# Performance work log

Measured on AMD Instinct MI355X. Metric: run time of the kernel, lower is better.

Reference implementation:

```python
import jax, jax.numpy as jnp
import numpy as np

DEPTH = 128
NEG_MAX = -jnp.finfo(jnp.float32).max


def setup_inputs() -> dict:
    key = jax.random.key(0)
    ks = jax.random.split(key, 10)
    B, S, F, C = 16, 2048, 512, 1000
    x = jax.random.normal(ks[0], (B, S, F), dtype=jnp.float32)
    attention_mask = jax.random.randint(ks[1], (B, S, S), 0, 2) == 1
    s = 1.0 / np.sqrt(F)
    Wq = jax.random.uniform(ks[2], (F, DEPTH), jnp.float32, -s, s)
    bq = jax.random.uniform(ks[3], (DEPTH,), jnp.float32, -s, s)
    Wk = jax.random.uniform(ks[4], (F, DEPTH), jnp.float32, -s, s)
    bk = jax.random.uniform(ks[5], (DEPTH,), jnp.float32, -s, s)
    Wv = jax.random.uniform(ks[6], (F, DEPTH), jnp.float32, -s, s)
    bv = jax.random.uniform(ks[7], (DEPTH,), jnp.float32, -s, s)
    sl = 1.0 / np.sqrt(DEPTH)
    Wl = jax.random.uniform(ks[8], (DEPTH, C), jnp.float32, -sl, sl)
    bl = jax.random.uniform(ks[9], (C,), jnp.float32, -sl, sl)
    return {"x": x, "attention_mask": attention_mask,
            "Wq": Wq, "bq": bq, "Wk": Wk, "bk": bk,
            "Wv": Wv, "bv": bv, "Wl": Wl, "bl": bl}


def reference(x, attention_mask, Wq, bq, Wk, bk, Wv, bv, Wl, bl):
    # x: [B, S, F]; single-head attention with depth=128
    q = (x @ Wq + bq) * (DEPTH ** -0.5)          # [B, S, D] (is_scaled_dot_product)
    k = x @ Wk + bk                               # [B, S, D]
    v = x @ Wv + bv                               # [B, S, D]
    logit = jnp.einsum('bsd,btd->bst', q, k)      # [B, S, S]
    # masked_fill_(mask, -float_max) then added to logits
    logit = logit + jnp.where(attention_mask, NEG_MAX, 0.0)
    attn = jax.nn.softmax(logit, axis=2)
    out = jnp.einsum('bst,btd->bsd', attn, v)     # [B, S, D]
    out = out @ Wl + bl                           # [B, S, C]
    return out.mean(axis=1)                       # [B, C]
```

## Files before the change

kernel.cpp:

```cpp
#include <hip/hip_runtime.h>
#include <stdint.h>

#define BB 16
#define SS 2048
#define FF 512
#define DD 128
#define CC 1000

typedef __attribute__((ext_vector_type(8))) short bf16x8;
typedef __attribute__((ext_vector_type(4))) float f32x4;

__device__ __forceinline__ unsigned short f2bf(float f) {
  unsigned x;
  __builtin_memcpy(&x, &f, 4);
  x = x + 0x7FFFu + ((x >> 16) & 1u);
  return (unsigned short)(x >> 16);
}
__device__ __forceinline__ float bf2f(unsigned short u) {
  unsigned x = ((unsigned)u) << 16;
  float f;
  __builtin_memcpy(&f, &x, 4);
  return f;
}
__device__ __forceinline__ unsigned pk2(float a, float b) {
  return (unsigned)f2bf(a) | ((unsigned)f2bf(b) << 16);
}

#define WS_WG   256
#define WS_PK   131328
#define WS_Q    8519936
#define WS_K    16908544
#define WS_V    25297152
#define WS_WT   33685760
#define WS_END  34078976

__global__ __launch_bounds__(256) void k_detect(const unsigned* __restrict__ mask,
                                                int* __restrict__ flags,
                                                float* __restrict__ wgl) {
  __shared__ unsigned red;
  const int tid = threadIdx.x;
  if (tid == 0) red = 0;
  __syncthreads();
  unsigned a = 0;
#pragma unroll
  for (int j = 0; j < 4; ++j) a |= mask[tid * 4 + j] & 0xFFFFFF00u;
  if (a) atomicOr(&red, 1u);
  __syncthreads();
  if (tid == 0) flags[0] = (red == 0) ? 1 : 0;
  for (int i = tid; i < BB * SS; i += 256) wgl[i] = 0.f;
}

__global__ __launch_bounds__(256) void k_pack(const void* __restrict__ mask,
                                              const int* __restrict__ flags,
                                              unsigned* __restrict__ pk) {
  const int tid = threadIdx.x;
  const long long base = (long long)blockIdx.x * 2048;
  const bool isInt = flags[0] != 0;
#pragma unroll
  for (int it = 0; it < 8; ++it) {
    long long e = base + it * 256 + tid;
    int val;
    if (isInt) val = ((const int*)mask)[e];
    else       val = ((const unsigned char*)mask)[e];
    unsigned long long bal = __ballot(val != 0);
    if ((tid & 31) == 0)
      pk[e >> 5] = (unsigned)((tid & 63) ? (bal >> 32) : bal);
  }
}

__global__ __launch_bounds__(256) void k_wt(const float* __restrict__ Wq,
                                            const float* __restrict__ Wk,
                                            const float* __restrict__ Wv,
                                            unsigned short* __restrict__ wt) {
  int idx = blockIdx.x * 256 + threadIdx.x;
  int ty = idx >> 16;
  int o = idx & 65535;
  int d = o >> 9, f = o & 511;
  const float* W = ty == 0 ? Wq : (ty == 1 ? Wk : Wv);
  wt[idx] = f2bf(W[f * DD + d]);
}

__global__ __launch_bounds__(256) void k_proj(const float* __restrict__ xg,
                                              const unsigned short* __restrict__ wtg,
                                              const float* __restrict__ bq,
                                              const float* __restrict__ bk,
                                              const float* __restrict__ bv,
                                              unsigned short* __restrict__ qo,
                                              unsigned short* __restrict__ ko,
                                              unsigned short* __restrict__ vo) {
  __shared__ __align__(16) char lA[8192];
  __shared__ __align__(16) char lB[8192];
  const int tid = threadIdx.x;
  const int lane = tid & 63;
  const int wv = tid >> 6;
  const int colL = lane & 15, quad = lane >> 4;
  const int blk = blockIdx.x, ty = blockIdx.y;
  const float* bias = ty == 0 ? bq : (ty == 1 ? bk : bv);
  unsigned short* outp = ty == 0 ? qo : (ty == 1 ? ko : vo);
  const float scale = ty == 0 ? 0.08838834764831845f : 1.0f;
  const unsigned short* wbase = wtg + (size_t)ty * 65536;
  const int m0 = (wv & 1) * 64, n0 = (wv >> 1) * 64;

  f32x4 acc[4][4];
  const f32x4 z4 = {0.f, 0.f, 0.f, 0.f};
#pragma unroll
  for (int mi = 0; mi < 4; ++mi)
#pragma unroll
    for (int ni = 0; ni < 4; ++ni) acc[mi][ni] = z4;

  for (int ic = 0; ic < 16; ++ic) {
    const int k0 = ic * 32;
    uint4 va[2], vb[2];
#pragma unroll
    for (int rr = 0; rr < 2; ++rr) {
      int p = rr * 256 + tid;
      int row = p >> 2, c = p & 3;
      const float* xp = xg + (size_t)(blk * 128 + row) * FF + k0 + c * 8;
      float4 x0 = *(const float4*)xp;
      float4 x1 = *(const float4*)(xp + 4);
      va[rr].x = pk2(x0.x, x0.y); va[rr].y = pk2(x0.z, x0.w);
      va[rr].z = pk2(x1.x, x1.y); va[rr].w = pk2(x1.z, x1.w);
      vb[rr] = *(const uint4*)(wbase + (size_t)row * FF + k0 + c * 8);
    }
    __syncthreads();
#pragma unroll
    for (int rr = 0; rr < 2; ++rr) {
      int p = rr * 256 + tid;
      int row = p >> 2, c = p & 3;
      int phys = c ^ ((row >> 1) & 3);
      *(uint4*)(lA + row * 64 + phys * 16) = va[rr];
      *(uint4*)(lB + row * 64 + phys * 16) = vb[rr];
    }
    __syncthreads();
    bf16x8 af[4], bfr[4];
#pragma unroll
    for (int mi = 0; mi < 4; ++mi) {
      int ar = m0 + mi * 16 + colL;
      int phys = quad ^ ((ar >> 1) & 3);
      af[mi] = *(const bf16x8*)(lA + ar * 64 + phys * 16);
    }
#pragma unroll
    for (int ni = 0; ni < 4; ++ni) {
      int br = n0 + ni * 16 + colL;
      int phys = quad ^ ((br >> 1) & 3);
      bfr[ni] = *(const bf16x8*)(lB + br * 64 + phys * 16);
    }
#pragma unroll
    for (int mi = 0; mi < 4; ++mi)
#pragma unroll
      for (int ni = 0; ni < 4; ++ni)
        acc[mi][ni] = __builtin_amdgcn_mfma_f32_16x16x32_bf16(af[mi], bfr[ni], acc[mi][ni], 0, 0, 0);
  }
#pragma unroll
  for (int ni = 0; ni < 4; ++ni) {
    int col = n0 + ni * 16 + colL;
    float bval = bias[col];
#pragma unroll
    for (int mi = 0; mi < 4; ++mi) {
#pragma unroll
      for (int r = 0; r < 4; ++r) {
        int row = blk * 128 + m0 + mi * 16 + quad * 4 + r;
        float val = (acc[mi][ni][r] + bval) * scale;
        outp[(size_t)row * DD + col] = f2bf(val);
      }
    }
  }
}

template <bool P1>
__device__ __forceinline__ void attn_tiles2(const char* kt, const unsigned* maskw,
                                            const bf16x8 (&qf)[2][4], float (&z)[2][4],
                                            const float (&zinv)[2][4], float* wacc,
                                            int t0, int colL, int quad, int wv) {
#pragma unroll
  for (int nt = 0; nt < 4; ++nt) {
    int rb = nt * 16 + colL;
    bf16x8 bb[4];
#pragma unroll
    for (int kk = 0; kk < 4; ++kk) {
      int phys = (kk * 4 + quad) ^ (rb & 7);
      bb[kk] = *(const bf16x8*)(kt + rb * 256 + phys * 16);
    }
    int tcol = t0 + nt * 16 + colL;
    int wword = tcol >> 5, wbit = tcol & 31;
    float cs = 0.f;
#pragma unroll
    for (int mi = 0; mi < 2; ++mi) {
      f32x4 acc = {0.f, 0.f, 0.f, 0.f};
      acc = __builtin_amdgcn_mfma_f32_16x16x32_bf16(qf[mi][0], bb[0], acc, 0, 0, 0);
      acc = __builtin_amdgcn_mfma_f32_16x16x32_bf16(qf[mi][1], bb[1], acc, 0, 0, 0);
      acc = __builtin_amdgcn_mfma_f32_16x16x32_bf16(qf[mi][2], bb[2], acc, 0, 0, 0);
      acc = __builtin_amdgcn_mfma_f32_16x16x32_bf16(qf[mi][3], bb[3], acc, 0, 0, 0);
      int rbase = wv * 32 + mi * 16 + quad * 4;
#pragma unroll
      for (int r = 0; r < 4; ++r) {
        unsigned mw = maskw[(rbase + r) * 64 + wword];
        float l = fminf(acc[r], 80.0f);
        float e = ((mw >> wbit) & 1u) ? 0.f : __expf(l);
        if (P1) z[mi][r] += e;
        else cs += e * zinv[mi][r];
      }
    }
    if (!P1) {
      cs += __shfl_xor(cs, 16, 64);
      cs += __shfl_xor(cs, 32, 64);
      if (quad == 0) atomicAdd(&wacc[tcol], cs);
    }
  }
}

__global__ __launch_bounds__(256) void k_attn(const unsigned short* __restrict__ qg,
                                              const unsigned short* __restrict__ kg,
                                              const unsigned* __restrict__ pk,
                                              float* __restrict__ wglob) {
  __shared__ __align__(16) char kt[16384];
  __shared__ __align__(16) unsigned maskw[8192];
  __shared__ float wacc[SS];
  const int tid = threadIdx.x;
  const int lane = tid & 63, wv = tid >> 6;
  const int colL = lane & 15, quad = lane >> 4;
  const int row0 = blockIdx.x * 128;
  const int b = blockIdx.y;

  for (int i = tid; i < SS; i += 256) wacc[i] = 0.f;
  {
    const uint4* src = (const uint4*)(pk + ((size_t)b * SS + row0) * 64);
    uint4* dst = (uint4*)maskw;
    for (int i = tid; i < 2048; i += 256) dst[i] = src[i];
  }
  bf16x8 qf[2][4];
#pragma unroll
  for (int mi = 0; mi < 2; ++mi) {
    int qrow = row0 + wv * 32 + mi * 16 + colL;
    const unsigned short* qp = qg + ((size_t)b * SS + qrow) * DD + quad * 8;
#pragma unroll
    for (int kk = 0; kk < 4; ++kk) qf[mi][kk] = *(const bf16x8*)(qp + kk * 32);
  }
  __syncthreads();

  float z[2][4] = {{0.f, 0.f, 0.f, 0.f}, {0.f, 0.f, 0.f, 0.f}};
  float zinv[2][4] = {{0.f, 0.f, 0.f, 0.f}, {0.f, 0.f, 0.f, 0.f}};

  for (int t0 = 0; t0 < SS; t0 += 64) {
    uint4 kreg[4];
#pragma unroll
    for (int rr = 0; rr < 4; ++rr) {
      int p = rr * 256 + tid;
      int row = p >> 4, c = p & 15;
      kreg[rr] = *(const uint4*)(kg + ((size_t)b * SS + t0 + row) * DD + c * 8);
    }
    __syncthreads();
#pragma unroll
    for (int rr = 0; rr < 4; ++rr) {
      int p = rr * 256 + tid;
      int row = p >> 4, c = p & 15;
      int phys = c ^ (row & 7);
      *(uint4*)(kt + row * 256 + phys * 16) = kreg[rr];
    }
    __syncthreads();
    attn_tiles2<true>(kt, maskw, qf, z, zinv, wacc, t0, colL, quad, wv);
  }
#pragma unroll
  for (int mi = 0; mi < 2; ++mi)
#pragma unroll
    for (int r = 0; r < 4; ++r) {
      float s = z[mi][r];
      s += __shfl_xor(s, 1, 64);
      s += __shfl_xor(s, 2, 64);
      s += __shfl_xor(s, 4, 64);
      s += __shfl_xor(s, 8, 64);
      zinv[mi][r] = 1.0f / fmaxf(s, 1e-30f);
    }
  for (int t0 = 0; t0 < SS; t0 += 64) {
    uint4 kreg[4];
#pragma unroll
    for (int rr = 0; rr < 4; ++rr) {
      int p = rr * 256 + tid;
      int row = p >> 4, c = p & 15;
      kreg[rr] = *(const uint4*)(kg + ((size_t)b * SS + t0 + row) * DD + c * 8);
    }
    __syncthreads();
#pragma unroll
    for (int rr = 0; rr < 4; ++rr) {
      int p = rr * 256 + tid;
      int row = p >> 4, c = p & 15;
      int phys = c ^ (row & 7);
      *(uint4*)(kt + row * 256 + phys * 16) = kreg[rr];
    }
    __syncthreads();
    attn_tiles2<false>(kt, maskw, qf, z, zinv, wacc, t0, colL, quad, wv);
  }
  __syncthreads();
  for (int i = tid; i < SS; i += 256)
    atomicAdd(&wglob[(size_t)b * SS + i], wacc[i]);
}

__global__ __launch_bounds__(256) void k_final(const float* __restrict__ wgl,
                                               const unsigned short* __restrict__ vg,
                                               const float* __restrict__ Wl,
                                               const float* __restrict__ bl,
                                               float* __restrict__ outp) {
  __shared__ float y[DD];
  __shared__ float tmp[DD];
  const int tid = threadIdx.x;
  const int b = blockIdx.x;
  const int d = tid & 127, half = tid >> 7;
  float p = 0.f;
  const float* wrow = wgl + (size_t)b * SS + half * 1024;
  const unsigned short* vrow = vg + ((size_t)b * SS + half * 1024) * DD + d;
#pragma unroll 8
  for (int t = 0; t < 1024; ++t) p += wrow[t] * bf2f(vrow[(size_t)t * DD]);
  if (half) tmp[d] = p;
  __syncthreads();
  if (!half) y[d] = (p + tmp[d]) * (1.0f / 2048.0f);
  __syncthreads();
  for (int c = tid; c < CC; c += 256) {
    float a = bl[c];
#pragma unroll 16
    for (int dd = 0; dd < DD; ++dd) a += y[dd] * Wl[dd * CC + c];
    outp[b * CC + c] = a;
  }
}

extern "C" void kernel_launch(void* const* d_in, const int* in_sizes, int n_in,
                              void* d_out, int out_size, void* d_ws, size_t ws_size,
                              hipStream_t stream) {
  const void* ptr[10];
  for (int i = 0; i < 10; ++i) ptr[i] = (i < n_in) ? d_in[i] : nullptr;
  if (n_in == 10) {
    const void *px = 0, *pm = 0, *pWl = 0, *pbl = 0;
    const void* pW[3] = {0, 0, 0};
    const void* pb[3] = {0, 0, 0};
    int nW = 0, nb = 0;
    for (int i = 0; i < 10; ++i) {
      int s = in_sizes[i];
      if (s == 16777216) px = d_in[i];
      else if (s == 67108864) pm = d_in[i];
      else if (s == 128000) pWl = d_in[i];
      else if (s == 1000) pbl = d_in[i];
      else if (s == 65536 && nW < 3) pW[nW++] = d_in[i];
      else if (s == 128 && nb < 3) pb[nb++] = d_in[i];
    }
    if (px && pm && pWl && pbl && nW == 3 && nb == 3) {
      ptr[0] = px; ptr[1] = pm;
      ptr[2] = pW[0]; ptr[3] = pb[0];
      ptr[4] = pW[1]; ptr[5] = pb[1];
      ptr[6] = pW[2]; ptr[7] = pb[2];
      ptr[8] = pWl; ptr[9] = pbl;
    }
  }
  char* ws = (char*)d_ws;
  if (ws_size < (size_t)WS_END) return;
  int* flags = (int*)ws;
  float* wg = (float*)(ws + WS_WG);
  unsigned* pk = (unsigned*)(ws + WS_PK);
  unsigned short* q  = (unsigned short*)(ws + WS_Q);
  unsigned short* k  = (unsigned short*)(ws + WS_K);
  unsigned short* v  = (unsigned short*)(ws + WS_V);
  unsigned short* wt = (unsigned short*)(ws + WS_WT);

  k_detect<<<1, 256, 0, stream>>>((const unsigned*)ptr[1], flags, wg);
  k_pack<<<32768, 256, 0, stream>>>(ptr[1], flags, pk);
  k_wt<<<768, 256, 0, stream>>>((const float*)ptr[2], (const float*)ptr[4],
                                (const float*)ptr[6], wt);
  k_proj<<<dim3(256, 3), 256, 0, stream>>>((const float*)ptr[0], wt,
                                           (const float*)ptr[3], (const float*)ptr[5],
                                           (const float*)ptr[7], q, k, v);
  k_attn<<<dim3(16, 16), 256, 0, stream>>>(q, k, pk, wg);
  k_final<<<16, 256, 0, stream>>>(wg, v, (const float*)ptr[8], (const float*)ptr[9],
                                  (float*)d_out);
}
```

Before: 687.5 us.

## Split attention over key chunks into two launches and parallelize final reduction

The single attention kernel that ran both softmax passes over all keys in 256 blocks is split into two kernels over a (row-block, key-chunk, batch) grid of 2048 blocks. The first accumulates row normalizers into global memory with atomics, and the second reads them and accumulates column weights. The weighted V reduction moves into its own kernel spread over 256 blocks with atomics, replacing the 16-block final kernel. This targets low occupancy on a large GPU, at the cost of extra launches, global atomics and reloading Q and mask tiles per chunk.

```diff
diff --git a/kernel.cpp b/kernel.cpp
--- a/kernel.cpp
+++ b/kernel.cpp
@@ -27,16 +27,20 @@
 }
 
 #define WS_WG   256
-#define WS_PK   131328
-#define WS_Q    8519936
-#define WS_K    16908544
-#define WS_V    25297152
-#define WS_WT   33685760
-#define WS_END  34078976
+#define WS_ZG   131328
+#define WS_YG   262400
+#define WS_PK   270592
+#define WS_Q    8659200
+#define WS_K    17047808
+#define WS_V    25436416
+#define WS_WT   33825024
+#define WS_END  34218240
 
 __global__ __launch_bounds__(256) void k_detect(const unsigned* __restrict__ mask,
                                                 int* __restrict__ flags,
-                                                float* __restrict__ wgl) {
+                                                float* __restrict__ wgl,
+                                                float* __restrict__ zgl,
+                                                float* __restrict__ ygl) {
   __shared__ unsigned red;
   const int tid = threadIdx.x;
   if (tid == 0) red = 0;
@@ -47,7 +51,8 @@
   if (a) atomicOr(&red, 1u);
   __syncthreads();
   if (tid == 0) flags[0] = (red == 0) ? 1 : 0;
-  for (int i = tid; i < BB * SS; i += 256) wgl[i] = 0.f;
+  for (int i = tid; i < BB * SS; i += 256) { wgl[i] = 0.f; zgl[i] = 0.f; }
+  for (int i = tid; i < BB * DD; i += 256) ygl[i] = 0.f;
 }
 
 __global__ __launch_bounds__(256) void k_pack(const void* __restrict__ mask,
@@ -167,67 +172,29 @@
   }
 }
 
-template <bool P1>
-__device__ __forceinline__ void attn_tiles2(const char* kt, const unsigned* maskw,
-                                            const bf16x8 (&qf)[2][4], float (&z)[2][4],
-                                            const float (&zinv)[2][4], float* wacc,
-                                            int t0, int colL, int quad, int wv) {
-#pragma unroll
-  for (int nt = 0; nt < 4; ++nt) {
-    int rb = nt * 16 + colL;
-    bf16x8 bb[4];
-#pragma unroll
-    for (int kk = 0; kk < 4; ++kk) {
-      int phys = (kk * 4 + quad) ^ (rb & 7);
-      bb[kk] = *(const bf16x8*)(kt + rb * 256 + phys * 16);
-    }
-    int tcol = t0 + nt * 16 + colL;
-    int wword = tcol >> 5, wbit = tcol & 31;
-    float cs = 0.f;
-#pragma unroll
-    for (int mi = 0; mi < 2; ++mi) {
-      f32x4 acc = {0.f, 0.f, 0.f, 0.f};
-      acc = __builtin_amdgcn_mfma_f32_16x16x32_bf16(qf[mi][0], bb[0], acc, 0, 0, 0);
-      acc = __builtin_amdgcn_mfma_f32_16x16x32_bf16(qf[mi][1], bb[1], acc, 0, 0, 0);
-      acc = __builtin_amdgcn_mfma_f32_16x16x32_bf16(qf[mi][2], bb[2], acc, 0, 0, 0);
-      acc = __builtin_amdgcn_mfma_f32_16x16x32_bf16(qf[mi][3], bb[3], acc, 0, 0, 0);
-      int rbase = wv * 32 + mi * 16 + quad * 4;
-#pragma unroll
-      for (int r = 0; r < 4; ++r) {
-        unsigned mw = maskw[(rbase + r) * 64 + wword];
-        float l = fminf(acc[r], 80.0f);
-        float e = ((mw >> wbit) & 1u) ? 0.f : __expf(l);
-        if (P1) z[mi][r] += e;
-        else cs += e * zinv[mi][r];
-      }
-    }
-    if (!P1) {
-      cs += __shfl_xor(cs, 16, 64);
-      cs += __shfl_xor(cs, 32, 64);
-      if (quad == 0) atomicAdd(&wacc[tcol], cs);
-    }
-  }
-}
-
-__global__ __launch_bounds__(256) void k_attn(const unsigned short* __restrict__ qg,
-                                              const unsigned short* __restrict__ kg,
-                                              const unsigned* __restrict__ pk,
-                                              float* __restrict__ wglob) {
+template <bool PZ>
+__global__ __launch_bounds__(256) void k_attn2(const unsigned short* __restrict__ qg,
+                                               const unsigned short* __restrict__ kg,
+                                               const unsigned* __restrict__ pk,
+                                               float* __restrict__ zg,
+                                               float* __restrict__ wg) {
   __shared__ __align__(16) char kt[16384];
-  __shared__ __align__(16) unsigned maskw[8192];
-  __shared__ float wacc[SS];
+  __shared__ unsigned maskt[128 * 9];
+  __shared__ float wacc[256];
   const int tid = threadIdx.x;
   const int lane = tid & 63, wv = tid >> 6;
   const int colL = lane & 15, quad = lane >> 4;
   const int row0 = blockIdx.x * 128;
-  const int b = blockIdx.y;
-
-  for (int i = tid; i < SS; i += 256) wacc[i] = 0.f;
-  {
-    const uint4* src = (const uint4*)(pk + ((size_t)b * SS + row0) * 64);
-    uint4* dst = (uint4*)maskw;
-    for (int i = tid; i < 2048; i += 256) dst[i] = src[i];
-  }
+  const int tc = blockIdx.y;
+  const int b = blockIdx.z;
+  const int tbase = tc * 256;
+
+  for (int i = tid; i < 1024; i += 256) {
+    int row = i >> 3, w = i & 7;
+    maskt[row * 9 + w] = pk[((size_t)b * SS + row0 + row) * 64 + tc * 8 + w];
+  }
+  if (!PZ) wacc[tid] = 0.f;
+
   bf16x8 qf[2][4];
 #pragma unroll
   for (int mi = 0; mi < 2; ++mi) {
@@ -236,12 +203,20 @@
 #pragma unroll
     for (int kk = 0; kk < 4; ++kk) qf[mi][kk] = *(const bf16x8*)(qp + kk * 32);
   }
-  __syncthreads();
-
   float z[2][4] = {{0.f, 0.f, 0.f, 0.f}, {0.f, 0.f, 0.f, 0.f}};
-  float zinv[2][4] = {{0.f, 0.f, 0.f, 0.f}, {0.f, 0.f, 0.f, 0.f}};
-
-  for (int t0 = 0; t0 < SS; t0 += 64) {
+  float zinv[2][4];
+  if (!PZ) {
+#pragma unroll
+    for (int mi = 0; mi < 2; ++mi)
+#pragma unroll
+      for (int r = 0; r < 4; ++r) {
+        int row = row0 + wv * 32 + mi * 16 + quad * 4 + r;
+        zinv[mi][r] = 1.0f / fmaxf(zg[(size_t)b * SS + row], 1e-30f);
+      }
+  }
+
+  for (int kt0 = 0; kt0 < 4; ++kt0) {
+    const int t0 = tbase + kt0 * 64;
     uint4 kreg[4];
 #pragma unroll
     for (int rr = 0; rr < 4; ++rr) {
@@ -258,66 +233,90 @@
       *(uint4*)(kt + row * 256 + phys * 16) = kreg[rr];
     }
     __syncthreads();
-    attn_tiles2<true>(kt, maskw, qf, z, zinv, wacc, t0, colL, quad, wv);
-  }
-#pragma unroll
-  for (int mi = 0; mi < 2; ++mi)
-#pragma unroll
-    for (int r = 0; r < 4; ++r) {
-      float s = z[mi][r];
-      s += __shfl_xor(s, 1, 64);
-      s += __shfl_xor(s, 2, 64);
-      s += __shfl_xor(s, 4, 64);
-      s += __shfl_xor(s, 8, 64);
-      zinv[mi][r] = 1.0f / fmaxf(s, 1e-30f);
-    }
-  for (int t0 = 0; t0 < SS; t0 += 64) {
-    uint4 kreg[4];
-#pragma unroll
-    for (int rr = 0; rr < 4; ++rr) {
-      int p = rr * 256 + tid;
-      int row = p >> 4, c = p & 15;
-      kreg[rr] = *(const uint4*)(kg + ((size_t)b * SS + t0 + row) * DD + c * 8);
-    }
-    __syncthreads();
-#pragma unroll
-    for (int rr = 0; rr < 4; ++rr) {
-      int p = rr * 256 + tid;
-      int row = p >> 4, c = p & 15;
-      int phys = c ^ (row & 7);
-      *(uint4*)(kt + row * 256 + phys * 16) = kreg[rr];
-    }
-    __syncthreads();
-    attn_tiles2<false>(kt, maskw, qf, z, zinv, wacc, t0, colL, quad, wv);
-  }
-  __syncthreads();
-  for (int i = tid; i < SS; i += 256)
-    atomicAdd(&wglob[(size_t)b * SS + i], wacc[i]);
-}
-
-__global__ __launch_bounds__(256) void k_final(const float* __restrict__ wgl,
-                                               const unsigned short* __restrict__ vg,
-                                               const float* __restrict__ Wl,
-                                               const float* __restrict__ bl,
-                                               float* __restrict__ outp) {
-  __shared__ float y[DD];
-  __shared__ float tmp[DD];
+#pragma unroll
+    for (int nt = 0; nt < 4; ++nt) {
+      int rb = nt * 16 + colL;
+      bf16x8 bb[4];
+#pragma unroll
+      for (int kk = 0; kk < 4; ++kk) {
+        int phys = (kk * 4 + quad) ^ (rb & 7);
+        bb[kk] = *(const bf16x8*)(kt + rb * 256 + phys * 16);
+      }
+      int tl = kt0 * 64 + nt * 16 + colL;
+      int wl = tl >> 5, wb = tl & 31;
+      float cs = 0.f;
+#pragma unroll
+      for (int mi = 0; mi < 2; ++mi) {
+        f32x4 acc = {0.f, 0.f, 0.f, 0.f};
+        acc = __builtin_amdgcn_mfma_f32_16x16x32_bf16(qf[mi][0], bb[0], acc, 0, 0, 0);
+        acc = __builtin_amdgcn_mfma_f32_16x16x32_bf16(qf[mi][1], bb[1], acc, 0, 0, 0);
+        acc = __builtin_amdgcn_mfma_f32_16x16x32_bf16(qf[mi][2], bb[2], acc, 0, 0, 0);
+        acc = __builtin_amdgcn_mfma_f32_16x16x32_bf16(qf[mi][3], bb[3], acc, 0, 0, 0);
+        int rbase = wv * 32 + mi * 16 + quad * 4;
+#pragma unroll
+        for (int r = 0; r < 4; ++r) {
+          unsigned mw = maskt[(rbase + r) * 9 + wl];
+          float e = ((mw >> wb) & 1u) ? 0.f : __expf(fminf(acc[r], 80.f));
+          if (PZ) z[mi][r] += e;
+          else cs += e * zinv[mi][r];
+        }
+      }
+      if (!PZ) {
+        cs += __shfl_xor(cs, 16, 64);
+        cs += __shfl_xor(cs, 32, 64);
+        if (quad == 0) atomicAdd(&wacc[tl], cs);
+      }
+    }
+  }
+  if (PZ) {
+#pragma unroll
+    for (int mi = 0; mi < 2; ++mi)
+#pragma unroll
+      for (int r = 0; r < 4; ++r) {
+        float s = z[mi][r];
+        s += __shfl_xor(s, 1, 64);
+        s += __shfl_xor(s, 2, 64);
+        s += __shfl_xor(s, 4, 64);
+        s += __shfl_xor(s, 8, 64);
+        if (colL == 0) {
+          int row = row0 + wv * 32 + mi * 16 + quad * 4 + r;
+          atomicAdd(&zg[(size_t)b * SS + row], s);
+        }
+      }
+  } else {
+    __syncthreads();
+    atomicAdd(&wg[(size_t)b * SS + tbase + tid], wacc[tid]);
+  }
+}
+
+__global__ __launch_bounds__(256) void k_yv(const float* __restrict__ wgl,
+                                            const unsigned short* __restrict__ vg,
+                                            float* __restrict__ ygl) {
+  const int tid = threadIdx.x;
+  const int tc = blockIdx.x, b = blockIdx.y;
+  const int d = tid & 127, half = tid >> 7;
+  const int t0 = tc * 128 + half * 64;
+  float p = 0.f;
+  const float* wrow = wgl + (size_t)b * SS + t0;
+  const unsigned short* vrow = vg + ((size_t)b * SS + t0) * DD + d;
+#pragma unroll 8
+  for (int t = 0; t < 64; ++t) p += wrow[t] * bf2f(vrow[(size_t)t * DD]);
+  atomicAdd(&ygl[b * DD + d], p);
+}
+
+__global__ __launch_bounds__(256) void k_out(const float* __restrict__ ygl,
+                                             const float* __restrict__ Wl,
+                                             const float* __restrict__ bl,
+                                             float* __restrict__ outp) {
+  __shared__ float ys[DD];
   const int tid = threadIdx.x;
   const int b = blockIdx.x;
-  const int d = tid & 127, half = tid >> 7;
-  float p = 0.f;
-  const float* wrow = wgl + (size_t)b * SS + half * 1024;
-  const unsigned short* vrow = vg + ((size_t)b * SS + half * 1024) * DD + d;
-#pragma unroll 8
-  for (int t = 0; t < 1024; ++t) p += wrow[t] * bf2f(vrow[(size_t)t * DD]);
-  if (half) tmp[d] = p;
-  __syncthreads();
-  if (!half) y[d] = (p + tmp[d]) * (1.0f / 2048.0f);
+  if (tid < DD) ys[tid] = ygl[b * DD + tid] * (1.0f / 2048.0f);
   __syncthreads();
   for (int c = tid; c < CC; c += 256) {
     float a = bl[c];
 #pragma unroll 16
-    for (int dd = 0; dd < DD; ++dd) a += y[dd] * Wl[dd * CC + c];
+    for (int dd = 0; dd < DD; ++dd) a += ys[dd] * Wl[dd * CC + c];
     outp[b * CC + c] = a;
   }
 }
@@ -353,20 +352,24 @@
   if (ws_size < (size_t)WS_END) return;
   int* flags = (int*)ws;
   float* wg = (float*)(ws + WS_WG);
+  float* zg = (float*)(ws + WS_ZG);
+  float* yg = (float*)(ws + WS_YG);
   unsigned* pk = (unsigned*)(ws + WS_PK);
   unsigned short* q  = (unsigned short*)(ws + WS_Q);
   unsigned short* k  = (unsigned short*)(ws + WS_K);
   unsigned short* v  = (unsigned short*)(ws + WS_V);
   unsigned short* wt = (unsigned short*)(ws + WS_WT);
 
-  k_detect<<<1, 256, 0, stream>>>((const unsigned*)ptr[1], flags, wg);
+  k_detect<<<1, 256, 0, stream>>>((const unsigned*)ptr[1], flags, wg, zg, yg);
   k_pack<<<32768, 256, 0, stream>>>(ptr[1], flags, pk);
   k_wt<<<768, 256, 0, stream>>>((const float*)ptr[2], (const float*)ptr[4],
                                 (const float*)ptr[6], wt);
   k_proj<<<dim3(256, 3), 256, 0, stream>>>((const float*)ptr[0], wt,
                                            (const float*)ptr[3], (const float*)ptr[5],
                                            (const float*)ptr[7], q, k, v);
-  k_attn<<<dim3(16, 16), 256, 0, stream>>>(q, k, pk, wg);
-  k_final<<<16, 256, 0, stream>>>(wg, v, (const float*)ptr[8], (const float*)ptr[9],
-                                  (float*)d_out);
-}
+  k_attn2<true><<<dim3(16, 8, 16), 256, 0, stream>>>(q, k, pk, zg, wg);
+  k_attn2<false><<<dim3(16, 8, 16), 256, 0, stream>>>(q, k, pk, zg, wg);
+  k_yv<<<dim3(16, 16), 256, 0, stream>>>(wg, v, yg);
+  k_out<<<16, 256, 0, stream>>>(yg, (const float*)ptr[8], (const float*)ptr[9],
+                                (float*)d_out);
+}
```

Result: faster. 611.2 us (-11.1%).
